# Performance work log

Measured on AMD Instinct MI355X. Metric: run time of the kernel, lower is better.

The kernel has to match this reference:

```python
import jax, jax.numpy as jnp
import numpy as np

N = 4096
VOCAB = 50257
EDIM = 1024
WFEAT = 1024
LABELS = 2
SLOPE = 0.01
NEG_INF = -1e9


def setup_inputs() -> dict:
    key = jax.random.key(0)
    ks = jax.random.split(key, 8)
    inSen = jax.random.randint(ks[0], (N,), 0, VOCAB, dtype=jnp.int64)
    adj = jax.random.randint(ks[1], (N, N), 0, 2, dtype=jnp.int32)
    emb_table = jax.random.normal(ks[2], (VOCAB, EDIM), dtype=jnp.float32) * 0.02
    W = jax.random.normal(ks[3], (EDIM, WFEAT), dtype=jnp.float32) * (1.0 / np.sqrt(EDIM))
    a_src = jax.random.normal(ks[4], (WFEAT,), dtype=jnp.float32) * (1.0 / np.sqrt(WFEAT))
    a_dst = jax.random.normal(ks[5], (WFEAT,), dtype=jnp.float32) * (1.0 / np.sqrt(WFEAT))
    clf_w = jax.random.normal(ks[6], (WFEAT, LABELS), dtype=jnp.float32) * (1.0 / np.sqrt(WFEAT))
    clf_b = jax.random.normal(ks[7], (LABELS,), dtype=jnp.float32) * 0.01
    return {"inSen": inSen, "adj": adj, "emb_table": emb_table, "W": W,
            "a_src": a_src, "a_dst": a_dst, "clf_w": clf_w, "clf_b": clf_b}


def reference(inSen, adj, emb_table, W, a_src, a_dst, clf_w, clf_b):
    # Embedding lookup: [N, edim]
    words = emb_table[inSen]
    # GAT layer: linear projection [N, wFeat]
    h = words @ W
    # Pairwise attention logits e_ij = LeakyReLU(a_src.h_i + a_dst.h_j)
    s_src = h @ a_src            # [N]
    s_dst = h @ a_dst            # [N]
    e = jax.nn.leaky_relu(s_src[:, None] + s_dst[None, :], negative_slope=SLOPE)  # [N, N]
    # Adjacency-masked softmax over neighbors (axis=1)
    e = jnp.where(adj > 0, e, NEG_INF)
    attention = jax.nn.softmax(e, axis=1)          # [N, N]
    sentence = attention @ h                       # [N, wFeat]
    # Mean pooling over nodes
    poolSentence = jnp.mean(sentence, axis=0)      # [wFeat]
    # Classifier + softmax over labels (dim=0 of a 1-D vector)
    label = jax.nn.softmax(poolSentence @ clf_w + clf_b, axis=0)  # [labels]
    return (poolSentence, attention, sentence, label)
```

## Files before the change

kernel.cpp:

```cpp
#include <hip/hip_runtime.h>
#include <hip/hip_bf16.h>

#define NN 4096
#define ED 1024
#define WF 1024
#define SLOPEC 0.01f
#define NEG_INFC -1e9f

typedef __attribute__((ext_vector_type(8))) short bf16x8;
typedef __attribute__((ext_vector_type(4))) short short4v;
typedef __attribute__((ext_vector_type(4))) float f32x4;
typedef __attribute__((ext_vector_type(4))) int int4v;

__device__ __forceinline__ float bf2f(short s) {
    union { unsigned u; float f; } v;
    v.u = ((unsigned)(unsigned short)s) << 16;
    return v.f;
}
__device__ __forceinline__ short f2bf(float f) {
    unsigned u = __float_as_uint(f);
    unsigned r = u + 0x7FFFu + ((u >> 16) & 1u);
    return (short)(r >> 16);
}

typedef __attribute__((address_space(3))) unsigned lds_u32;
typedef const __attribute__((address_space(1))) unsigned gbl_u32;
__device__ __forceinline__ void g2l16(const short* g, short* l) {
    __builtin_amdgcn_global_load_lds((gbl_u32*)g, (lds_u32*)l, 16, 0, 0);
}

__global__ __launch_bounds__(256) void k_prep(const float* __restrict__ W,
                                              short* __restrict__ Wt,
                                              const int* __restrict__ inSen,
                                              const float* __restrict__ emb,
                                              short* __restrict__ X,
                                              float* __restrict__ zbase) {
    if (blockIdx.x < 256) {
        if (blockIdx.x < 9) {
            f32x4 z = {0.f, 0.f, 0.f, 0.f};
            *(f32x4*)(zbase + blockIdx.x * 1024 + threadIdx.x * 4) = z;
        }
        __shared__ float t[64][65];
        const int n0 = (blockIdx.x & 15) * 64, k0 = (blockIdx.x >> 4) * 64;
        const int tx = threadIdx.x & 63, ty = threadIdx.x >> 6;
#pragma unroll
        for (int p = 0; p < 16; p++) {
            int r = p * 4 + ty;
            t[r][tx] = W[(long)(k0 + r) * WF + n0 + tx];
        }
        __syncthreads();
#pragma unroll
        for (int p = 0; p < 16; p++) {
            int r = p * 4 + ty;
            Wt[(long)(n0 + r) * ED + k0 + tx] = f2bf(t[tx][r]);
        }
    } else {
        const int row = blockIdx.x - 256;
        const int tid = threadIdx.x;
        const long idx = inSen[row];
        const float4 v = ((const float4*)(emb + idx * ED))[tid];
        short4v s;
        s.x = f2bf(v.x); s.y = f2bf(v.y); s.z = f2bf(v.z); s.w = f2bf(v.w);
        *(short4v*)(X + (long)row * ED + tid * 4) = s;
    }
}

template <int BM, int BN, int MODE, bool SWAPXY>
__global__ __launch_bounds__(256, 2) void gemm_bt2(
    const short* __restrict__ A, const short* __restrict__ Bt,
    int N, int K, int Kc, void* __restrict__ Cout,
    const float* __restrict__ a_src, const float* __restrict__ a_dst,
    float* __restrict__ s_src, float* __restrict__ s_dst,
    float* __restrict__ pool) {
    constexpr int TM = BM / 32;
    constexpr int TN = BN / 32;
    constexpr int STAGE = (BM + BN) * 128;
    constexpr int SMEMSZ = (MODE == 0 && BM * BN > STAGE) ? BM * BN : STAGE;
    __shared__ __align__(16) short smem[SMEMSZ];
    short* sA = smem;
    short* sB = smem + BM * 128;

    const int tid = threadIdx.x;
    const int lane = tid & 63;
    const int wid = tid >> 6;
    const int wm = wid >> 1, wn = wid & 1;
    const int n0 = (SWAPXY ? blockIdx.y : blockIdx.x) * BN;
    const int m0 = (SWAPXY ? blockIdx.x : blockIdx.y) * BM;
    const int ks = blockIdx.z * Kc;

    const int srow = tid >> 2;
    const int sc8 = (tid & 3) * 8;
    const int l15 = lane & 15;
    const int lhi = lane >> 4;

    f32x4 acc[TM][TN];
#pragma unroll
    for (int t = 0; t < TM; t++)
#pragma unroll
        for (int u = 0; u < TN; u++) acc[t][u] = (f32x4){0.f, 0.f, 0.f, 0.f};

    const short* Ab = A + (long)(m0 + srow) * K + ks + sc8;
    const short* Bb = Bt + (long)(n0 + srow) * K + ks + sc8;
    const long rstep = (long)64 * K;

    for (int k0 = 0; k0 < Kc; k0 += 128) {
#pragma unroll
        for (int c = 0; c < 4; c++) {
#pragma unroll
            for (int p = 0; p < BM / 64; p++)
                g2l16(Ab + p * rstep + k0 + c * 32,
                      sA + c * (BM * 32) + (p * 256 + wid * 64) * 8);
#pragma unroll
            for (int p = 0; p < BN / 64; p++)
                g2l16(Bb + p * rstep + k0 + c * 32,
                      sB + c * (BN * 32) + (p * 256 + wid * 64) * 8);
        }
        __syncthreads();

#pragma unroll
        for (int c = 0; c < 4; c++) {
            bf16x8 af[TM], bfr[TN];
#pragma unroll
            for (int t = 0; t < TM; t++)
                af[t] = *(const bf16x8*)&sA[c * (BM * 32) +
                        (wm * (BM / 2) + t * 16 + l15) * 32 + lhi * 8];
#pragma unroll
            for (int u = 0; u < TN; u++)
                bfr[u] = *(const bf16x8*)&sB[c * (BN * 32) +
                         (wn * (BN / 2) + u * 16 + l15) * 32 + lhi * 8];
#pragma unroll
            for (int t = 0; t < TM; t++)
#pragma unroll
                for (int u = 0; u < TN; u++)
                    acc[t][u] = __builtin_amdgcn_mfma_f32_16x16x32_bf16(
                        af[t], bfr[u], acc[t][u], 0, 0, 0);
        }
        __syncthreads();
    }

    if (MODE == 0) {
        short* sT = smem;
#pragma unroll
        for (int t = 0; t < TM; t++)
#pragma unroll
            for (int u = 0; u < TN; u++)
#pragma unroll
                for (int r = 0; r < 4; r++) {
                    int m = wm * (BM / 2) + t * 16 + lhi * 4 + r;
                    int n = wn * (BN / 2) + u * 16 + l15;
                    sT[m * BN + n] = f2bf(acc[t][u][r]);
                }
        __syncthreads();
        short* C = (short*)Cout;
#pragma unroll
        for (int q = 0; q < BM * BN / 2048; q++) {
            int idx = q * 256 + tid;
            int row = idx / (BN / 8);
            int c8 = (idx % (BN / 8)) * 8;
            *(bf16x8*)(C + (long)(m0 + row) * N + n0 + c8) =
                *(const bf16x8*)&sT[row * BN + c8];
        }
        float ps[TN], pd[TN];
#pragma unroll
        for (int u = 0; u < TN; u++) { ps[u] = 0.f; pd[u] = 0.f; }
#pragma unroll
        for (int t = 0; t < TM; t++)
#pragma unroll
            for (int r = 0; r < 4; r++) {
                int m = m0 + wm * (BM / 2) + t * 16 + lhi * 4 + r;
                float as = a_src[m], ad = a_dst[m];
#pragma unroll
                for (int u = 0; u < TN; u++) {
                    ps[u] += acc[t][u][r] * as;
                    pd[u] += acc[t][u][r] * ad;
                }
            }
#pragma unroll
        for (int u = 0; u < TN; u++) {
            ps[u] += __shfl_xor(ps[u], 16); ps[u] += __shfl_xor(ps[u], 32);
            pd[u] += __shfl_xor(pd[u], 16); pd[u] += __shfl_xor(pd[u], 32);
        }
        if (lane < 16) {
#pragma unroll
            for (int u = 0; u < TN; u++) {
                int n = n0 + wn * (BN / 2) + u * 16 + lane;
                atomicAdd(s_src + n, ps[u]);
                atomicAdd(s_dst + n, pd[u]);
            }
        }
    } else {
        float* C = (float*)Cout;
        float pp[TN];
#pragma unroll
        for (int u = 0; u < TN; u++) pp[u] = 0.f;
#pragma unroll
        for (int t = 0; t < TM; t++)
#pragma unroll
            for (int u = 0; u < TN; u++)
#pragma unroll
                for (int r = 0; r < 4; r++) {
                    int m = wm * (BM / 2) + t * 16 + lhi * 4 + r;
                    int n = wn * (BN / 2) + u * 16 + l15;
                    C[(long)(m0 + m) * N + n0 + n] = acc[t][u][r];
                    pp[u] += acc[t][u][r];
                }
#pragma unroll
        for (int u = 0; u < TN; u++) {
            pp[u] += __shfl_xor(pp[u], 16);
            pp[u] += __shfl_xor(pp[u], 32);
        }
        if (lane < 16) {
#pragma unroll
            for (int u = 0; u < TN; u++) {
                int n = n0 + wn * (BN / 2) + u * 16 + lane;
                atomicAdd(pool + n, pp[u]);
            }
        }
    }
}

__global__ __launch_bounds__(256) void k_attn(const int* __restrict__ adj,
                                              const float* __restrict__ s_src,
                                              const float* __restrict__ s_dst,
                                              float* __restrict__ attn,
                                              short* __restrict__ attnB) {
    __shared__ float wred[4];
    __shared__ float wred2[4];
    const int row = blockIdx.x;
    const int tid = threadIdx.x;
    const float ss = s_src[row];
    const int4v* adj4 = (const int4v*)(adj + (long)row * NN);
    const f32x4* sd4 = (const f32x4*)s_dst;
    float v[16];
    float vmax = -3e38f;
#pragma unroll
    for (int c = 0; c < 4; c++) {
        int idx = c * 256 + tid;
        int4v a = __builtin_nontemporal_load(&adj4[idx]);
        f32x4 d = sd4[idx];
        float x0 = ss + d.x; x0 = x0 > 0.f ? x0 : SLOPEC * x0; x0 = a.x > 0 ? x0 : NEG_INFC;
        float x1 = ss + d.y; x1 = x1 > 0.f ? x1 : SLOPEC * x1; x1 = a.y > 0 ? x1 : NEG_INFC;
        float x2 = ss + d.z; x2 = x2 > 0.f ? x2 : SLOPEC * x2; x2 = a.z > 0 ? x2 : NEG_INFC;
        float x3 = ss + d.w; x3 = x3 > 0.f ? x3 : SLOPEC * x3; x3 = a.w > 0 ? x3 : NEG_INFC;
        v[c * 4 + 0] = x0; v[c * 4 + 1] = x1; v[c * 4 + 2] = x2; v[c * 4 + 3] = x3;
        vmax = fmaxf(vmax, fmaxf(fmaxf(x0, x1), fmaxf(x2, x3)));
    }
#pragma unroll
    for (int off = 32; off; off >>= 1) vmax = fmaxf(vmax, __shfl_xor(vmax, off));
    if ((tid & 63) == 0) wred[tid >> 6] = vmax;
    __syncthreads();
    vmax = fmaxf(fmaxf(wred[0], wred[1]), fmaxf(wred[2], wred[3]));

    float sum = 0.f;
#pragma unroll
    for (int c = 0; c < 16; c++) {
        v[c] = __expf(v[c] - vmax);
        sum += v[c];
    }
#pragma unroll
    for (int off = 32; off; off >>= 1) sum += __shfl_xor(sum, off);
    if ((tid & 63) == 0) wred2[tid >> 6] = sum;
    __syncthreads();
    sum = wred2[0] + wred2[1] + wred2[2] + wred2[3];
    const float inv = 1.0f / sum;

    f32x4* o4 = (f32x4*)(attn + (long)row * NN);
    short4v* b4 = (short4v*)(attnB + (long)row * NN);
#pragma unroll
    for (int c = 0; c < 4; c++) {
        int idx = c * 256 + tid;
        f32x4 o;
        o.x = v[c * 4 + 0] * inv; o.y = v[c * 4 + 1] * inv;
        o.z = v[c * 4 + 2] * inv; o.w = v[c * 4 + 3] * inv;
        __builtin_nontemporal_store(o, &o4[idx]);
        short4v sb;
        sb.x = f2bf(o.x); sb.y = f2bf(o.y); sb.z = f2bf(o.z); sb.w = f2bf(o.w);
        b4[idx] = sb;
    }
}

__global__ __launch_bounds__(256) void k_final(const float* __restrict__ pool_acc,
                                               const float* __restrict__ clf_w,
                                               const float* __restrict__ clf_b,
                                               float* __restrict__ out_pool,
                                               float* __restrict__ out_label) {
    __shared__ float r0[4], r1[4];
    const int tid = threadIdx.x;
    float l0 = 0.f, l1 = 0.f;
#pragma unroll
    for (int q = 0; q < 4; q++) {
        int f = q * 256 + tid;
        float p = pool_acc[f] * (1.0f / NN);
        out_pool[f] = p;
        l0 += p * clf_w[f * 2 + 0];
        l1 += p * clf_w[f * 2 + 1];
    }
#pragma unroll
    for (int off = 32; off; off >>= 1) {
        l0 += __shfl_xor(l0, off);
        l1 += __shfl_xor(l1, off);
    }
    if ((tid & 63) == 0) { r0[tid >> 6] = l0; r1[tid >> 6] = l1; }
    __syncthreads();
    if (tid == 0) {
        float L0 = r0[0] + r0[1] + r0[2] + r0[3] + clf_b[0];
        float L1 = r1[0] + r1[1] + r1[2] + r1[3] + clf_b[1];
        float m = fmaxf(L0, L1);
        float e0 = __expf(L0 - m), e1 = __expf(L1 - m);
        float s = e0 + e1;
        out_label[0] = e0 / s;
        out_label[1] = e1 / s;
    }
}

extern "C" void kernel_launch(void* const* d_in, const int* in_sizes, int n_in,
                              void* d_out, int out_size, void* d_ws,
                              size_t ws_size, hipStream_t stream) {
    const int* inSen = (const int*)d_in[0];
    const int* adj = (const int*)d_in[1];
    const float* emb = (const float*)d_in[2];
    const float* W = (const float*)d_in[3];
    const float* a_src = (const float*)d_in[4];
    const float* a_dst = (const float*)d_in[5];
    const float* clf_w = (const float*)d_in[6];
    const float* clf_b = (const float*)d_in[7];

    float* out = (float*)d_out;
    float* out_pool = out;
    float* attn = out + 1024;
    float* sentence = out + 1024 + (long)NN * NN;
    float* out_label = out + 1024 + (long)NN * NN + (long)NN * WF;

    char* ws = (char*)d_ws;
    short* X = (short*)ws;
    short* Wt = (short*)(ws + (8l << 20));
    short* Ht = (short*)(ws + (10l << 20));
    short* attnB = (short*)(ws + (18l << 20));
    float* s_src = (float*)(ws + (52l << 20));
    float* s_dst = s_src + NN;
    float* pool = s_dst + NN;

    k_prep<<<256 + NN, 256, 0, stream>>>(W, Wt, inSen, emb, X, s_src);

    gemm_bt2<64, 128, 0, false><<<dim3(NN / 128, WF / 64, 1), 256, 0, stream>>>(
        Wt, X, NN, ED, ED, Ht, a_src, a_dst, s_src, s_dst, nullptr);

    k_attn<<<NN, 256, 0, stream>>>(adj, s_src, s_dst, attn, attnB);

    gemm_bt2<64, 128, 1, true><<<dim3(NN / 64, WF / 128, 1), 256, 0, stream>>>(
        attnB, Ht, WF, NN, NN, sentence,
        nullptr, nullptr, nullptr, nullptr, pool);

    k_final<<<1, 256, 0, stream>>>(pool, clf_w, clf_b, out_pool, out_label);
}
```

Before: 387.1 us.

## Precompute W·a score vectors and co-schedule projection GEMM with attention softmax

The attention scores are now computed as X·(W·a) instead of reducing over the projected features. The vectors W·a_src and W·a_dst are built inside the weight-transpose prep kernel, and a small score kernel then computes them per row. This removes the dependency between the projection GEMM and the attention softmax, so both now run as two block ranges of one fused launch. The GEMM uses a smaller K-step tile so it fits more blocks per CU. The price is an extra memset and an extra launch, plus atomics and a slightly different rounding path, since the scores come from bf16 X rather than fp32 h.

```diff
diff --git a/kernel.cpp b/kernel.cpp
--- a/kernel.cpp
+++ b/kernel.cpp
@@ -34,11 +34,15 @@
                                               const int* __restrict__ inSen,
                                               const float* __restrict__ emb,
                                               short* __restrict__ X,
-                                              float* __restrict__ zbase) {
+                                              const float* __restrict__ a_src,
+                                              const float* __restrict__ a_dst,
+                                              float* __restrict__ v_src,
+                                              float* __restrict__ v_dst,
+                                              float* __restrict__ pool) {
     if (blockIdx.x < 256) {
-        if (blockIdx.x < 9) {
+        if (blockIdx.x == 0) {
             f32x4 z = {0.f, 0.f, 0.f, 0.f};
-            *(f32x4*)(zbase + blockIdx.x * 1024 + threadIdx.x * 4) = z;
+            *(f32x4*)(pool + threadIdx.x * 4) = z;
         }
         __shared__ float t[64][65];
         const int n0 = (blockIdx.x & 15) * 64, k0 = (blockIdx.x >> 4) * 64;
@@ -53,6 +57,20 @@
         for (int p = 0; p < 16; p++) {
             int r = p * 4 + ty;
             Wt[(long)(n0 + r) * ED + k0 + tx] = f2bf(t[tx][r]);
+        }
+        const int r = threadIdx.x >> 2, q = threadIdx.x & 3;
+        float pvs = 0.f, pvd = 0.f;
+#pragma unroll
+        for (int j = 0; j < 16; j++) {
+            float w = t[r][q * 16 + j];
+            pvs += w * a_src[n0 + q * 16 + j];
+            pvd += w * a_dst[n0 + q * 16 + j];
+        }
+        pvs += __shfl_xor(pvs, 1); pvs += __shfl_xor(pvs, 2);
+        pvd += __shfl_xor(pvd, 1); pvd += __shfl_xor(pvd, 2);
+        if (q == 0) {
+            atomicAdd(v_src + k0 + r, pvs);
+            atomicAdd(v_dst + k0 + r, pvd);
         }
     } else {
         const int row = blockIdx.x - 256;
@@ -65,80 +83,97 @@
     }
 }
 
-template <int BM, int BN, int MODE, bool SWAPXY>
-__global__ __launch_bounds__(256, 2) void gemm_bt2(
-    const short* __restrict__ A, const short* __restrict__ Bt,
-    int N, int K, int Kc, void* __restrict__ Cout,
-    const float* __restrict__ a_src, const float* __restrict__ a_dst,
-    float* __restrict__ s_src, float* __restrict__ s_dst,
-    float* __restrict__ pool) {
-    constexpr int TM = BM / 32;
-    constexpr int TN = BN / 32;
-    constexpr int STAGE = (BM + BN) * 128;
-    constexpr int SMEMSZ = (MODE == 0 && BM * BN > STAGE) ? BM * BN : STAGE;
-    __shared__ __align__(16) short smem[SMEMSZ];
-    short* sA = smem;
-    short* sB = smem + BM * 128;
-
+__global__ __launch_bounds__(256) void k_score(const short* __restrict__ X,
+                                               const float* __restrict__ v_src,
+                                               const float* __restrict__ v_dst,
+                                               float* __restrict__ s_src,
+                                               float* __restrict__ s_dst) {
+    const int wid = threadIdx.x >> 6, lane = threadIdx.x & 63;
+    const int row = blockIdx.x * 4 + wid;
+    const short* xr = X + (long)row * ED + lane * 16;
+    bf16x8 a0 = *(const bf16x8*)xr;
+    bf16x8 a1 = *(const bf16x8*)(xr + 8);
+    const float* vs = v_src + lane * 16;
+    const float* vd = v_dst + lane * 16;
+    float ss = 0.f, sd = 0.f;
+#pragma unroll
+    for (int j = 0; j < 8; j++) {
+        float x0 = bf2f(a0[j]), x1 = bf2f(a1[j]);
+        ss += x0 * vs[j] + x1 * vs[8 + j];
+        sd += x0 * vd[j] + x1 * vd[8 + j];
+    }
+#pragma unroll
+    for (int off = 32; off; off >>= 1) {
+        ss += __shfl_xor(ss, off);
+        sd += __shfl_xor(sd, off);
+    }
+    if (lane == 0) { s_src[row] = ss; s_dst[row] = sd; }
+}
+
+__global__ __launch_bounds__(256, 4) void k_fused(
+    const short* __restrict__ Wt, const short* __restrict__ X,
+    short* __restrict__ Ht,
+    const int* __restrict__ adj,
+    const float* __restrict__ s_src, const float* __restrict__ s_dst,
+    float* __restrict__ attn, short* __restrict__ attnB) {
+    __shared__ __align__(16) short smem[12288];
+    const int b = blockIdx.x;
     const int tid = threadIdx.x;
-    const int lane = tid & 63;
-    const int wid = tid >> 6;
-    const int wm = wid >> 1, wn = wid & 1;
-    const int n0 = (SWAPXY ? blockIdx.y : blockIdx.x) * BN;
-    const int m0 = (SWAPXY ? blockIdx.x : blockIdx.y) * BM;
-    const int ks = blockIdx.z * Kc;
-
-    const int srow = tid >> 2;
-    const int sc8 = (tid & 3) * 8;
-    const int l15 = lane & 15;
-    const int lhi = lane >> 4;
-
-    f32x4 acc[TM][TN];
-#pragma unroll
-    for (int t = 0; t < TM; t++)
-#pragma unroll
-        for (int u = 0; u < TN; u++) acc[t][u] = (f32x4){0.f, 0.f, 0.f, 0.f};
-
-    const short* Ab = A + (long)(m0 + srow) * K + ks + sc8;
-    const short* Bb = Bt + (long)(n0 + srow) * K + ks + sc8;
-    const long rstep = (long)64 * K;
-
-    for (int k0 = 0; k0 < Kc; k0 += 128) {
-#pragma unroll
-        for (int c = 0; c < 4; c++) {
-#pragma unroll
-            for (int p = 0; p < BM / 64; p++)
-                g2l16(Ab + p * rstep + k0 + c * 32,
-                      sA + c * (BM * 32) + (p * 256 + wid * 64) * 8);
-#pragma unroll
-            for (int p = 0; p < BN / 64; p++)
-                g2l16(Bb + p * rstep + k0 + c * 32,
-                      sB + c * (BN * 32) + (p * 256 + wid * 64) * 8);
-        }
-        __syncthreads();
-
-#pragma unroll
-        for (int c = 0; c < 4; c++) {
-            bf16x8 af[TM], bfr[TN];
-#pragma unroll
-            for (int t = 0; t < TM; t++)
-                af[t] = *(const bf16x8*)&sA[c * (BM * 32) +
-                        (wm * (BM / 2) + t * 16 + l15) * 32 + lhi * 8];
-#pragma unroll
-            for (int u = 0; u < TN; u++)
-                bfr[u] = *(const bf16x8*)&sB[c * (BN * 32) +
-                         (wn * (BN / 2) + u * 16 + l15) * 32 + lhi * 8];
-#pragma unroll
-            for (int t = 0; t < TM; t++)
+
+    if (b < 512) {
+        constexpr int BM = 64, BN = 128, TM = 2, TN = 4;
+        short* sA = smem;
+        short* sB = smem + BM * 64;
+        const int lane = tid & 63;
+        const int wid = tid >> 6;
+        const int wm = wid >> 1, wn = wid & 1;
+        const int n0 = (b & 31) * BN;
+        const int m0 = (b >> 5) * BM;
+        const int srow = tid >> 2;
+        const int sc8 = (tid & 3) * 8;
+        const int l15 = lane & 15;
+        const int lhi = lane >> 4;
+
+        f32x4 acc[TM][TN];
+#pragma unroll
+        for (int t = 0; t < TM; t++)
+#pragma unroll
+            for (int u = 0; u < TN; u++) acc[t][u] = (f32x4){0.f, 0.f, 0.f, 0.f};
+
+        const short* Ab = Wt + (long)(m0 + srow) * ED + sc8;
+        const short* Bb = X + (long)(n0 + srow) * ED + sc8;
+        const long rstep = (long)64 * ED;
+
+        for (int k0 = 0; k0 < ED; k0 += 64) {
+#pragma unroll
+            for (int c = 0; c < 2; c++) {
+                g2l16(Ab + k0 + c * 32, sA + c * (BM * 32) + (wid * 64) * 8);
+#pragma unroll
+                for (int p = 0; p < 2; p++)
+                    g2l16(Bb + p * rstep + k0 + c * 32,
+                          sB + c * (BN * 32) + (p * 256 + wid * 64) * 8);
+            }
+            __syncthreads();
+#pragma unroll
+            for (int c = 0; c < 2; c++) {
+                bf16x8 af[TM], bfr[TN];
+#pragma unroll
+                for (int t = 0; t < TM; t++)
+                    af[t] = *(const bf16x8*)&sA[c * (BM * 32) +
+                            (wm * (BM / 2) + t * 16 + l15) * 32 + lhi * 8];
 #pragma unroll
                 for (int u = 0; u < TN; u++)
-                    acc[t][u] = __builtin_amdgcn_mfma_f32_16x16x32_bf16(
-                        af[t], bfr[u], acc[t][u], 0, 0, 0);
-        }
-        __syncthreads();
-    }
-
-    if (MODE == 0) {
+                    bfr[u] = *(const bf16x8*)&sB[c * (BN * 32) +
+                             (wn * (BN / 2) + u * 16 + l15) * 32 + lhi * 8];
+#pragma unroll
+                for (int t = 0; t < TM; t++)
+#pragma unroll
+                    for (int u = 0; u < TN; u++)
+                        acc[t][u] = __builtin_amdgcn_mfma_f32_16x16x32_bf16(
+                            af[t], bfr[u], acc[t][u], 0, 0, 0);
+            }
+            __syncthreads();
+        }
         short* sT = smem;
 #pragma unroll
         for (int t = 0; t < TM; t++)
@@ -151,131 +186,163 @@
                     sT[m * BN + n] = f2bf(acc[t][u][r]);
                 }
         __syncthreads();
-        short* C = (short*)Cout;
 #pragma unroll
         for (int q = 0; q < BM * BN / 2048; q++) {
             int idx = q * 256 + tid;
             int row = idx / (BN / 8);
             int c8 = (idx % (BN / 8)) * 8;
-            *(bf16x8*)(C + (long)(m0 + row) * N + n0 + c8) =
+            *(bf16x8*)(Ht + (long)(m0 + row) * NN + n0 + c8) =
                 *(const bf16x8*)&sT[row * BN + c8];
         }
-        float ps[TN], pd[TN];
-#pragma unroll
-        for (int u = 0; u < TN; u++) { ps[u] = 0.f; pd[u] = 0.f; }
-#pragma unroll
-        for (int t = 0; t < TM; t++)
+    } else {
+        float* wred = (float*)smem;
+        float* wred2 = (float*)smem + 4;
+        const int row = b - 512;
+        const float ss = s_src[row];
+        const int4v* adj4 = (const int4v*)(adj + (long)row * NN);
+        const f32x4* sd4 = (const f32x4*)s_dst;
+        float v[16];
+        float vmax = -3e38f;
+#pragma unroll
+        for (int c = 0; c < 4; c++) {
+            int idx = c * 256 + tid;
+            int4v a = __builtin_nontemporal_load(&adj4[idx]);
+            f32x4 d = sd4[idx];
+            float x0 = ss + d.x; x0 = x0 > 0.f ? x0 : SLOPEC * x0; x0 = a.x > 0 ? x0 : NEG_INFC;
+            float x1 = ss + d.y; x1 = x1 > 0.f ? x1 : SLOPEC * x1; x1 = a.y > 0 ? x1 : NEG_INFC;
+            float x2 = ss + d.z; x2 = x2 > 0.f ? x2 : SLOPEC * x2; x2 = a.z > 0 ? x2 : NEG_INFC;
+            float x3 = ss + d.w; x3 = x3 > 0.f ? x3 : SLOPEC * x3; x3 = a.w > 0 ? x3 : NEG_INFC;
+            v[c * 4 + 0] = x0; v[c * 4 + 1] = x1; v[c * 4 + 2] = x2; v[c * 4 + 3] = x3;
+            vmax = fmaxf(vmax, fmaxf(fmaxf(x0, x1), fmaxf(x2, x3)));
+        }
+#pragma unroll
+        for (int off = 32; off; off >>= 1) vmax = fmaxf(vmax, __shfl_xor(vmax, off));
+        if ((tid & 63) == 0) wred[tid >> 6] = vmax;
+        __syncthreads();
+        vmax = fmaxf(fmaxf(wred[0], wred[1]), fmaxf(wred[2], wred[3]));
+
+        float sum = 0.f;
+#pragma unroll
+        for (int c = 0; c < 16; c++) {
+            v[c] = __expf(v[c] - vmax);
+            sum += v[c];
+        }
+#pragma unroll
+        for (int off = 32; off; off >>= 1) sum += __shfl_xor(sum, off);
+        if ((tid & 63) == 0) wred2[tid >> 6] = sum;
+        __syncthreads();
+        sum = wred2[0] + wred2[1] + wred2[2] + wred2[3];
+        const float inv = 1.0f / sum;
+
+        f32x4* o4 = (f32x4*)(attn + (long)row * NN);
+        short4v* b4 = (short4v*)(attnB + (long)row * NN);
+#pragma unroll
+        for (int c = 0; c < 4; c++) {
+            int idx = c * 256 + tid;
+            f32x4 o;
+            o.x = v[c * 4 + 0] * inv; o.y = v[c * 4 + 1] * inv;
+            o.z = v[c * 4 + 2] * inv; o.w = v[c * 4 + 3] * inv;
+            __builtin_nontemporal_store(o, &o4[idx]);
+            short4v sb;
+            sb.x = f2bf(o.x); sb.y = f2bf(o.y); sb.z = f2bf(o.z); sb.w = f2bf(o.w);
+            b4[idx] = sb;
+        }
+    }
+}
+
+template <int BM, int BN>
+__global__ __launch_bounds__(256, 2) void gemm_bt2(
+    const short* __restrict__ A, const short* __restrict__ Bt,
+    int N, int K, void* __restrict__ Cout,
+    float* __restrict__ pool) {
+    constexpr int TM = BM / 32;
+    constexpr int TN = BN / 32;
+    __shared__ __align__(16) short smem[(BM + BN) * 128];
+    short* sA = smem;
+    short* sB = smem + BM * 128;
+
+    const int tid = threadIdx.x;
+    const int lane = tid & 63;
+    const int wid = tid >> 6;
+    const int wm = wid >> 1, wn = wid & 1;
+    const int n0 = blockIdx.y * BN;
+    const int m0 = blockIdx.x * BM;
+
+    const int srow = tid >> 2;
+    const int sc8 = (tid & 3) * 8;
+    const int l15 = lane & 15;
+    const int lhi = lane >> 4;
+
+    f32x4 acc[TM][TN];
+#pragma unroll
+    for (int t = 0; t < TM; t++)
+#pragma unroll
+        for (int u = 0; u < TN; u++) acc[t][u] = (f32x4){0.f, 0.f, 0.f, 0.f};
+
+    const short* Ab = A + (long)(m0 + srow) * K + sc8;
+    const short* Bb = Bt + (long)(n0 + srow) * K + sc8;
+    const long rstep = (long)64 * K;
+
+    for (int k0 = 0; k0 < K; k0 += 128) {
+#pragma unroll
+        for (int c = 0; c < 4; c++) {
+#pragma unroll
+            for (int p = 0; p < BM / 64; p++)
+                g2l16(Ab + p * rstep + k0 + c * 32,
+                      sA + c * (BM * 32) + (p * 256 + wid * 64) * 8);
+#pragma unroll
+            for (int p = 0; p < BN / 64; p++)
+                g2l16(Bb + p * rstep + k0 + c * 32,
+                      sB + c * (BN * 32) + (p * 256 + wid * 64) * 8);
+        }
+        __syncthreads();
+#pragma unroll
+        for (int c = 0; c < 4; c++) {
+            bf16x8 af[TM], bfr[TN];
+#pragma unroll
+            for (int t = 0; t < TM; t++)
+                af[t] = *(const bf16x8*)&sA[c * (BM * 32) +
+                        (wm * (BM / 2) + t * 16 + l15) * 32 + lhi * 8];
+#pragma unroll
+            for (int u = 0; u < TN; u++)
+                bfr[u] = *(const bf16x8*)&sB[c * (BN * 32) +
+                         (wn * (BN / 2) + u * 16 + l15) * 32 + lhi * 8];
+#pragma unroll
+            for (int t = 0; t < TM; t++)
+#pragma unroll
+                for (int u = 0; u < TN; u++)
+                    acc[t][u] = __builtin_amdgcn_mfma_f32_16x16x32_bf16(
+                        af[t], bfr[u], acc[t][u], 0, 0, 0);
+        }
+        __syncthreads();
+    }
+
+    float* C = (float*)Cout;
+    float pp[TN];
+#pragma unroll
+    for (int u = 0; u < TN; u++) pp[u] = 0.f;
+#pragma unroll
+    for (int t = 0; t < TM; t++)
+#pragma unroll
+        for (int u = 0; u < TN; u++)
 #pragma unroll
             for (int r = 0; r < 4; r++) {
-                int m = m0 + wm * (BM / 2) + t * 16 + lhi * 4 + r;
-                float as = a_src[m], ad = a_dst[m];
-#pragma unroll
-                for (int u = 0; u < TN; u++) {
-                    ps[u] += acc[t][u][r] * as;
-                    pd[u] += acc[t][u][r] * ad;
-                }
+                int m = wm * (BM / 2) + t * 16 + lhi * 4 + r;
+                int n = wn * (BN / 2) + u * 16 + l15;
+                C[(long)(m0 + m) * N + n0 + n] = acc[t][u][r];
+                pp[u] += acc[t][u][r];
             }
 #pragma unroll
+    for (int u = 0; u < TN; u++) {
+        pp[u] += __shfl_xor(pp[u], 16);
+        pp[u] += __shfl_xor(pp[u], 32);
+    }
+    if (lane < 16) {
+#pragma unroll
         for (int u = 0; u < TN; u++) {
-            ps[u] += __shfl_xor(ps[u], 16); ps[u] += __shfl_xor(ps[u], 32);
-            pd[u] += __shfl_xor(pd[u], 16); pd[u] += __shfl_xor(pd[u], 32);
-        }
-        if (lane < 16) {
-#pragma unroll
-            for (int u = 0; u < TN; u++) {
-                int n = n0 + wn * (BN / 2) + u * 16 + lane;
-                atomicAdd(s_src + n, ps[u]);
-                atomicAdd(s_dst + n, pd[u]);
-            }
-        }
-    } else {
-        float* C = (float*)Cout;
-        float pp[TN];
-#pragma unroll
-        for (int u = 0; u < TN; u++) pp[u] = 0.f;
-#pragma unroll
-        for (int t = 0; t < TM; t++)
-#pragma unroll
-            for (int u = 0; u < TN; u++)
-#pragma unroll
-                for (int r = 0; r < 4; r++) {
-                    int m = wm * (BM / 2) + t * 16 + lhi * 4 + r;
-                    int n = wn * (BN / 2) + u * 16 + l15;
-                    C[(long)(m0 + m) * N + n0 + n] = acc[t][u][r];
-                    pp[u] += acc[t][u][r];
-                }
-#pragma unroll
-        for (int u = 0; u < TN; u++) {
-            pp[u] += __shfl_xor(pp[u], 16);
-            pp[u] += __shfl_xor(pp[u], 32);
-        }
-        if (lane < 16) {
-#pragma unroll
-            for (int u = 0; u < TN; u++) {
-                int n = n0 + wn * (BN / 2) + u * 16 + lane;
-                atomicAdd(pool + n, pp[u]);
-            }
-        }
-    }
-}
-
-__global__ __launch_bounds__(256) void k_attn(const int* __restrict__ adj,
-                                              const float* __restrict__ s_src,
-                                              const float* __restrict__ s_dst,
-                                              float* __restrict__ attn,
-                                              short* __restrict__ attnB) {
-    __shared__ float wred[4];
-    __shared__ float wred2[4];
-    const int row = blockIdx.x;
-    const int tid = threadIdx.x;
-    const float ss = s_src[row];
-    const int4v* adj4 = (const int4v*)(adj + (long)row * NN);
-    const f32x4* sd4 = (const f32x4*)s_dst;
-    float v[16];
-    float vmax = -3e38f;
-#pragma unroll
-    for (int c = 0; c < 4; c++) {
-        int idx = c * 256 + tid;
-        int4v a = __builtin_nontemporal_load(&adj4[idx]);
-        f32x4 d = sd4[idx];
-        float x0 = ss + d.x; x0 = x0 > 0.f ? x0 : SLOPEC * x0; x0 = a.x > 0 ? x0 : NEG_INFC;
-        float x1 = ss + d.y; x1 = x1 > 0.f ? x1 : SLOPEC * x1; x1 = a.y > 0 ? x1 : NEG_INFC;
-        float x2 = ss + d.z; x2 = x2 > 0.f ? x2 : SLOPEC * x2; x2 = a.z > 0 ? x2 : NEG_INFC;
-        float x3 = ss + d.w; x3 = x3 > 0.f ? x3 : SLOPEC * x3; x3 = a.w > 0 ? x3 : NEG_INFC;
-        v[c * 4 + 0] = x0; v[c * 4 + 1] = x1; v[c * 4 + 2] = x2; v[c * 4 + 3] = x3;
-        vmax = fmaxf(vmax, fmaxf(fmaxf(x0, x1), fmaxf(x2, x3)));
-    }
-#pragma unroll
-    for (int off = 32; off; off >>= 1) vmax = fmaxf(vmax, __shfl_xor(vmax, off));
-    if ((tid & 63) == 0) wred[tid >> 6] = vmax;
-    __syncthreads();
-    vmax = fmaxf(fmaxf(wred[0], wred[1]), fmaxf(wred[2], wred[3]));
-
-    float sum = 0.f;
-#pragma unroll
-    for (int c = 0; c < 16; c++) {
-        v[c] = __expf(v[c] - vmax);
-        sum += v[c];
-    }
-#pragma unroll
-    for (int off = 32; off; off >>= 1) sum += __shfl_xor(sum, off);
-    if ((tid & 63) == 0) wred2[tid >> 6] = sum;
-    __syncthreads();
-    sum = wred2[0] + wred2[1] + wred2[2] + wred2[3];
-    const float inv = 1.0f / sum;
-
-    f32x4* o4 = (f32x4*)(attn + (long)row * NN);
-    short4v* b4 = (short4v*)(attnB + (long)row * NN);
-#pragma unroll
-    for (int c = 0; c < 4; c++) {
-        int idx = c * 256 + tid;
-        f32x4 o;
-        o.x = v[c * 4 + 0] * inv; o.y = v[c * 4 + 1] * inv;
-        o.z = v[c * 4 + 2] * inv; o.w = v[c * 4 + 3] * inv;
-        __builtin_nontemporal_store(o, &o4[idx]);
-        short4v sb;
-        sb.x = f2bf(o.x); sb.y = f2bf(o.y); sb.z = f2bf(o.z); sb.w = f2bf(o.w);
-        b4[idx] = sb;
+            int n = n0 + wn * (BN / 2) + u * 16 + lane;
+            atomicAdd(pool + n, pp[u]);
+        }
     }
 }
 
@@ -339,17 +406,21 @@
     float* s_src = (float*)(ws + (52l << 20));
     float* s_dst = s_src + NN;
     float* pool = s_dst + NN;
-
-    k_prep<<<256 + NN, 256, 0, stream>>>(W, Wt, inSen, emb, X, s_src);
-
-    gemm_bt2<64, 128, 0, false><<<dim3(NN / 128, WF / 64, 1), 256, 0, stream>>>(
-        Wt, X, NN, ED, ED, Ht, a_src, a_dst, s_src, s_dst, nullptr);
-
-    k_attn<<<NN, 256, 0, stream>>>(adj, s_src, s_dst, attn, attnB);
-
-    gemm_bt2<64, 128, 1, true><<<dim3(NN / 64, WF / 128, 1), 256, 0, stream>>>(
-        attnB, Ht, WF, NN, NN, sentence,
-        nullptr, nullptr, nullptr, nullptr, pool);
+    float* v_src = pool + WF;
+    float* v_dst = v_src + ED;
+
+    (void)hipMemsetAsync(v_src, 0, 2 * ED * sizeof(float), stream);
+
+    k_prep<<<256 + NN, 256, 0, stream>>>(W, Wt, inSen, emb, X,
+                                         a_src, a_dst, v_src, v_dst, pool);
+
+    k_score<<<NN / 4, 256, 0, stream>>>(X, v_src, v_dst, s_src, s_dst);
+
+    k_fused<<<512 + NN, 256, 0, stream>>>(Wt, X, Ht, adj, s_src, s_dst,
+                                          attn, attnB);
+
+    gemm_bt2<64, 128><<<dim3(NN / 64, WF / 128, 1), 256, 0, stream>>>(
+        attnB, Ht, WF, NN, sentence, pool);
 
     k_final<<<1, 256, 0, stream>>>(pool, clf_w, clf_b, out_pool, out_label);
 }
```

After: 389.6 us. Within noise of the previous version (+0.6%).
